# Optimization experiments

Hardware: AMD Instinct MI355X
Metric: run time of the kernel (lower is better)

## Reference

```python
import jax, jax.numpy as jnp
import numpy as np
from jax import lax

C = 256        # shared head channels (out_ch)
NB = 6         # anchors per spatial location
NC = 9         # num_classes (incl. background)
B = 16         # batch
FM = [(38, 38), (19, 19), (10, 10), (5, 5), (3, 3), (1, 1)]
BIAS_PRIOR = -float(np.log((1.0 - 0.01) / 0.01))  # focal-style prior on cls bias


def _conv(x, w, b):
    # 3x3 conv, stride 1, SAME padding, NCHW/OIHW
    y = lax.conv_general_dilated(x, w, (1, 1), 'SAME',
                                 dimension_numbers=('NCHW', 'OIHW', 'NCHW'))
    return y + b[None, :, None, None]


def _head(x, ws, bs):
    for w, b in zip(ws[:-1], bs[:-1]):
        x = jax.nn.relu(_conv(x, w, b))
    return _conv(x, ws[-1], bs[-1])


def setup_inputs() -> dict:
    key = jax.random.key(0)
    ks = jax.random.split(key, 20)
    d = {}
    for i, (h, w) in enumerate(FM):
        d[f'feat{i}'] = jax.random.normal(ks[i], (B, C, h, w), dtype=jnp.float32)
    for i in range(4):
        d[f'rw{i}'] = 0.01 * jax.random.normal(ks[6 + i], (C, C, 3, 3), dtype=jnp.float32)
        d[f'rb{i}'] = jnp.zeros((C,), jnp.float32)
    d['rw4'] = 0.01 * jax.random.normal(ks[10], (NB * 4, C, 3, 3), dtype=jnp.float32)
    d['rb4'] = jnp.zeros((NB * 4,), jnp.float32)
    for i in range(4):
        d[f'cw{i}'] = 0.01 * jax.random.normal(ks[11 + i], (C, C, 3, 3), dtype=jnp.float32)
        d[f'cb{i}'] = jnp.zeros((C,), jnp.float32)
    d['cw4'] = 0.01 * jax.random.normal(ks[15], (NB * NC, C, 3, 3), dtype=jnp.float32)
    cb4 = jnp.zeros((NB * NC,), jnp.float32)
    d['cb4'] = cb4.at[:NB].set(BIAS_PRIOR)  # bias_per_class = n_boxes entries
    return d


def reference(feat0, feat1, feat2, feat3, feat4, feat5,
              rw0, rw1, rw2, rw3, rw4, rb0, rb1, rb2, rb3, rb4,
              cw0, cw1, cw2, cw3, cw4, cb0, cb1, cb2, cb3, cb4):
    feats = [feat0, feat1, feat2, feat3, feat4, feat5]
    rws = [rw0, rw1, rw2, rw3, rw4]
    rbs = [rb0, rb1, rb2, rb3, rb4]
    cws = [cw0, cw1, cw2, cw3, cw4]
    cbs = [cb0, cb1, cb2, cb3, cb4]
    locs, confs = [], []
    for x in feats:
        n = x.shape[0]
        locs.append(_head(x, rws, rbs).reshape(n, 4, -1))       # [N,4,NB*H*W]
        confs.append(_head(x, cws, cbs).reshape(n, NC, -1))     # [N,NC,NB*H*W]
    bbox_delta = jnp.concatenate(locs, axis=2)   # [N, 4, total_anchors]
    confidences = jnp.concatenate(confs, axis=2)  # [N, NC, total_anchors]
    return bbox_delta, confidences
```

## Files before the change

kernel.cpp:

```cpp
#include <hip/hip_runtime.h>
#include <hip/hip_bf16.h>

typedef __attribute__((ext_vector_type(8))) __bf16 bf16x8;
typedef __attribute__((ext_vector_type(4))) float f32x4;

__device__ __forceinline__ unsigned short f2bf(float f) {
    unsigned int u = __float_as_uint(f);
    u += 0x7fff + ((u >> 16) & 1);
    return (unsigned short)(u >> 16);
}

__device__ __forceinline__ void gload16(const void* g, void* l) {
    __builtin_amdgcn_global_load_lds(
        (const __attribute__((address_space(1))) void*)g,
        (__attribute__((address_space(3))) void*)l, 16, 0, 0);
}

#define ZOFFB (31040 * 512)

__device__ __forceinline__ void tile256(int rt, int& rb, int& dim, int& row0) {
    if (rt < 91)       { rb = 0;     dim = 38; row0 = rt * 256; }
    else if (rt < 114) { rb = 23104; dim = 19; row0 = (rt - 91) * 256; }
    else if (rt < 121) { rb = 28880; dim = 10; row0 = (rt - 114) * 256; }
    else if (rt < 123) { rb = 30480; dim = 5;  row0 = (rt - 121) * 256; }
    else if (rt < 124) { rb = 30880; dim = 3;  row0 = (rt - 123) * 256; }
    else               { rb = 31024; dim = 1;  row0 = 0; }
    row0 += rb;
}

__device__ __forceinline__ void tile128(int rt, int& rb, int& dim, int& row0, int& aoff) {
    if (rt < 181)      { rb = 0;     dim = 38; row0 = rt * 128;         aoff = 0;     }
    else if (rt < 227) { rb = 23104; dim = 19; row0 = (rt - 181) * 128; aoff = 8664;  }
    else if (rt < 240) { rb = 28880; dim = 10; row0 = (rt - 227) * 128; aoff = 10830; }
    else if (rt < 244) { rb = 30480; dim = 5;  row0 = (rt - 240) * 128; aoff = 11430; }
    else if (rt < 246) { rb = 30880; dim = 3;  row0 = (rt - 244) * 128; aoff = 11580; }
    else               { rb = 31024; dim = 1;  row0 = (rt - 246) * 128; aoff = 11634; }
    row0 += rb;
}

struct WT { const float* src[10]; };
__global__ __launch_bounds__(256) void wtrans_all(WT wt, unsigned short* __restrict__ Wb,
                                                  unsigned short* __restrict__ WF) {
    int cr = blockIdx.x;
    int ci = threadIdx.x;
    const float* src;
    unsigned short* dst;
    int co, Cout;
    if (cr < 2048) {
        int slot = cr >> 8; co = cr & 255;
        src = wt.src[slot];
        dst = Wb + (size_t)slot * 589824 + (size_t)co * 2304;
        Cout = 256;
    } else {
        int r = cr - 2048;
        int slot = r >> 6; co = r & 63;
        src = wt.src[8 + slot];
        dst = WF + (size_t)slot * 147456 + (size_t)co * 2304;
        Cout = slot ? 54 : 24;
    }
    float v[9];
    if (co < Cout) {
        const float* s = src + (size_t)(co * 256 + ci) * 9;
#pragma unroll
        for (int t = 0; t < 9; ++t) v[t] = s[t];
    } else {
#pragma unroll
        for (int t = 0; t < 9; ++t) v[t] = 0.0f;
    }
#pragma unroll
    for (int t = 0; t < 9; ++t) dst[t * 256 + ci] = f2bf(v[t]);
}

struct FT { const float* src[6]; unsigned short* halo[4]; int nh; };
__global__ void ftrans_all(FT ft, unsigned short* __restrict__ X0) {
    int idx = blockIdx.x * 256 + threadIdx.x;
    if (idx >= 993280) {
        int idx2 = idx - 993280;
        int buf = idx2 >> 8, off = idx2 & 255;
        if (buf < ft.nh) ft.halo[buf][off] = 0;
        return;
    }
    int row = idx >> 5;
    int c8  = (idx & 31) << 3;
    int m, rb, dim;
    if (row < 23104)      { m = 0; rb = 0;     dim = 38; }
    else if (row < 28880) { m = 1; rb = 23104; dim = 19; }
    else if (row < 30480) { m = 2; rb = 28880; dim = 10; }
    else if (row < 30880) { m = 3; rb = 30480; dim = 5;  }
    else if (row < 31024) { m = 4; rb = 30880; dim = 3;  }
    else                  { m = 5; rb = 31024; dim = 1;  }
    int HW = dim * dim;
    int rel = row - rb;
    int b = rel / HW;
    int hw = rel - b * HW;
    const float* s = ft.src[m] + (size_t)(b * 256 + c8) * HW + hw;
    union { unsigned short u[8]; uint4 v; } tmp;
#pragma unroll
    for (int j = 0; j < 8; ++j) tmp.u[j] = f2bf(s[(size_t)j * HW]);
    *reinterpret_cast<uint4*>(X0 + ((size_t)row << 8) + c8) = tmp.v;
}

struct GArgs {
    const unsigned short* X[2];
    const unsigned short* W[2];
    const float* B[2];
    unsigned short* Y[2];
};

__global__ __launch_bounds__(512, 2) void conv_gemm(GArgs ga) {
    __shared__ unsigned char As[65536];
    __shared__ unsigned char Bs[65536];

    const int hz = blockIdx.y;
    const unsigned char* __restrict__ Xb = (const unsigned char*)ga.X[hz];
    const unsigned char* __restrict__ Wt = (const unsigned char*)ga.W[hz];
    const float* __restrict__ bias = ga.B[hz];
    unsigned short* __restrict__ Y = ga.Y[hz];

    int rb, dim, row0;
    tile256(blockIdx.x, rb, dim, row0);
    const int HWm = dim * dim;
    const int rowEnd = rb + 16 * HWm;

    const int tid = threadIdx.x;
    const int lane = tid & 63, wid = tid >> 6;
    const int lr = lane & 15, lg = lane >> 4;
    const int wm = wid >> 2, wn = wid & 3;

    const int sr0 = tid >> 2;
    const int xsw = (((tid & 3) ^ ((sr0 >> 1) & 3)) << 4);
    const unsigned char* Zr = Xb + ZOFFB + xsw;

    int gg[2], ay[2], ax[2];
    bool av[2];
#pragma unroll
    for (int it = 0; it < 2; ++it) {
        int g = row0 + sr0 + it * 128;
        bool v = g < rowEnd;
        int rel = v ? (g - rb) : 0;
        int b = rel / HWm;
        int hw = rel - b * HWm;
        int y = hw / dim;
        gg[it] = g; ay[it] = y; ax[it] = hw - y * dim; av[it] = v;
    }

    const unsigned char* bsrc0 = Wt + (size_t)sr0 * 4608 + xsw;
    const unsigned char* bsrc1 = Wt + (size_t)(sr0 + 128) * 4608 + xsw;

    auto tapA = [&](int tap, const unsigned char*& p0, const unsigned char*& p1) {
        int q3 = tap / 3;
        int dy = q3 - 1, dx = tap - q3 * 3 - 1;
        int ddd = dy * dim + dx;
        bool v0 = av[0] && ((unsigned)(ay[0] + dy) < (unsigned)dim) && ((unsigned)(ax[0] + dx) < (unsigned)dim);
        bool v1 = av[1] && ((unsigned)(ay[1] + dy) < (unsigned)dim) && ((unsigned)(ax[1] + dx) < (unsigned)dim);
        p0 = v0 ? Xb + (size_t)(gg[0] + ddd) * 512 + xsw : Zr;
        p1 = v1 ? Xb + (size_t)(gg[1] + ddd) * 512 + xsw : Zr;
    };

    const int fswz = ((lg ^ ((lr >> 1) & 3)) << 4);
    const int aRd = (wm * 128 + lr) * 64 + fswz;
    const int bRd = (wn * 64 + lr) * 64 + fswz;
    const int dSt = wid * 1024;

    f32x4 acc[8][4];
#pragma unroll
    for (int i = 0; i < 8; ++i)
#pragma unroll
        for (int j = 0; j < 4; ++j) acc[i][j] = (f32x4){0.f, 0.f, 0.f, 0.f};

    const unsigned char *aC0, *aC1, *aN0, *aN1;
    tapA(0, aC0, aC1);
#pragma unroll
    for (int kt = 0; kt < 3; ++kt) {
        gload16(aC0 + kt * 64, As + kt * 16384 + dSt);
        gload16(aC1 + kt * 64, As + kt * 16384 + 8192 + dSt);
        gload16(bsrc0 + kt * 64, Bs + kt * 16384 + dSt);
        gload16(bsrc1 + kt * 64, Bs + kt * 16384 + 8192 + dSt);
    }

#pragma unroll 1
    for (int tap = 0; tap < 9; ++tap) {
        if (tap < 8) tapA(tap + 1, aN0, aN1);
        else { aN0 = Zr; aN1 = Zr; }
        const unsigned char* bT0 = bsrc0 + tap * 512;
        const unsigned char* bT1 = bsrc1 + tap * 512;

#pragma unroll
        for (int kc = 0; kc < 8; ++kc) {
            const int bufc = kc & 3;
            const int bufs = (kc + 3) & 3;

            asm volatile("s_waitcnt vmcnt(8)" ::: "memory");
            __builtin_amdgcn_s_barrier();
            asm volatile("" ::: "memory");

            {
                const unsigned char *sa0, *sa1, *sb0, *sb1;
                if (kc < 5) {
                    sa0 = aC0 + (kc + 3) * 64; sa1 = aC1 + (kc + 3) * 64;
                    sb0 = bT0 + (kc + 3) * 64; sb1 = bT1 + (kc + 3) * 64;
                } else {
                    sa0 = aN0 + (kc - 5) * 64; sa1 = aN1 + (kc - 5) * 64;
                    sb0 = bT0 + 512 + (kc - 5) * 64; sb1 = bT1 + 512 + (kc - 5) * 64;
                }
                gload16(sa0, As + bufs * 16384 + dSt);
                gload16(sa1, As + bufs * 16384 + 8192 + dSt);
                gload16(sb0, Bs + bufs * 16384 + dSt);
                gload16(sb1, Bs + bufs * 16384 + 8192 + dSt);
            }

            const unsigned char* ab = As + bufc * 16384;
            const unsigned char* bb = Bs + bufc * 16384;
            bf16x8 rA[8], rB[4];
#pragma unroll
            for (int j = 0; j < 4; ++j) rB[j] = *(const bf16x8*)(bb + bRd + j * 1024);
#pragma unroll
            for (int i = 0; i < 8; ++i) rA[i] = *(const bf16x8*)(ab + aRd + i * 1024);
#pragma unroll
            for (int i = 0; i < 8; ++i)
#pragma unroll
                for (int j = 0; j < 4; ++j)
                    acc[i][j] = __builtin_amdgcn_mfma_f32_16x16x32_bf16(rA[i], rB[j], acc[i][j], 0, 0, 0);
        }
        aC0 = aN0; aC1 = aN1;
    }

    float bj[4];
#pragma unroll
    for (int j = 0; j < 4; ++j) bj[j] = bias[wn * 64 + j * 16 + lr];
#pragma unroll
    for (int i = 0; i < 8; ++i) {
        int rbase = row0 + wm * 128 + i * 16 + lg * 4;
#pragma unroll
        for (int rr = 0; rr < 4; ++rr) {
            int orow = rbase + rr;
            if (orow < rowEnd) {
                size_t yb = (size_t)orow * 256 + wn * 64 + lr;
#pragma unroll
                for (int j = 0; j < 4; ++j) {
                    float v = acc[i][j][rr] + bj[j];
                    Y[yb + j * 16] = f2bf(fmaxf(v, 0.f));
                }
            }
        }
    }
}

struct FArgs {
    const unsigned short* X[2];
    const unsigned short* W[2];
    const float* B[2];
    float* out;
    int hbase;
};

__global__ __launch_bounds__(256) void conv_final(FArgs fa) {
    __shared__ unsigned char As[32768];
    __shared__ unsigned char Bs[16384];

    const int zi = blockIdx.z;
    const int hz = zi + fa.hbase;
    const unsigned char* Xb = (const unsigned char*)fa.X[zi];
    const unsigned char* Wt = (const unsigned char*)fa.W[zi];
    const float* bias = fa.B[zi];
    float* out = fa.out;

    int rb, dim, row0, aoff;
    tile128(blockIdx.x, rb, dim, row0, aoff);
    const int HWm = dim * dim;
    const int rowEnd = rb + 16 * HWm;

    const int tid = threadIdx.x;
    const int lane = tid & 63, wid = tid >> 6;
    const int lr = lane & 15, lg = lane >> 4;

    const int swz16 = (((lane & 3) ^ ((lane >> 3) & 3)) << 4);
    const int srow = wid * 16 + (lane >> 2);
    const unsigned char* Zr = Xb + ZOFFB + swz16;

    int ay[2], ax[2], arel[2];
    bool av0[2];
#pragma unroll
    for (int it = 0; it < 2; ++it) {
        int r = row0 + it * 64 + srow;
        bool v = r < rowEnd;
        int rel = v ? (r - rb) : 0;
        int b = rel / HWm;
        int hw = rel - b * HWm;
        int y = hw / dim;
        ay[it] = y; ax[it] = hw - y * dim; arel[it] = rel; av0[it] = v;
    }

    const unsigned char* bB = Wt + (size_t)srow * 4608 + swz16;

    const int fsw = ((lg ^ ((lr >> 1) & 3)) << 4);
    const int aRd = (wid * 32 + lr) * 64 + fsw;
    const int bRd = lr * 64 + fsw;
    const int dA0 = wid * 1024;

    f32x4 acc[2][4];
#pragma unroll
    for (int i = 0; i < 2; ++i)
#pragma unroll
        for (int j = 0; j < 4; ++j) acc[i][j] = (f32x4){0.f, 0.f, 0.f, 0.f};

    auto tapPtr = [&](int tap, const unsigned char** aP) {
        int q3 = tap / 3;
        int dy = q3 - 1, dx = tap - q3 * 3 - 1;
#pragma unroll
        for (int it = 0; it < 2; ++it) {
            bool v = av0[it] && ((unsigned)(ay[it] + dy) < (unsigned)dim)
                             && ((unsigned)(ax[it] + dx) < (unsigned)dim);
            int off = v ? (rb + arel[it] + dy * dim + dx) * 512 : ZOFFB;
            aP[it] = Xb + off + swz16;
        }
    };

    const unsigned char* aP[2];
    const unsigned char* aPn[2];
    tapPtr(0, aP);
#pragma unroll
    for (int kt = 0; kt < 3; ++kt) {
        gload16(aP[0] + kt * 64, As + kt * 8192 + dA0);
        gload16(aP[1] + kt * 64, As + kt * 8192 + 4096 + dA0);
        gload16(bB + kt * 64, Bs + kt * 4096 + dA0);
    }

#pragma unroll 1
    for (int tap = 0; tap < 9; ++tap) {
        if (tap < 8) tapPtr(tap + 1, aPn);
        else { aPn[0] = Zr; aPn[1] = Zr; }
        const unsigned char* bP = bB + tap * 512;

#pragma unroll
        for (int kin = 0; kin < 8; ++kin) {
            const int sc = kin & 3;
            const int ss = (kin + 3) & 3;

            asm volatile("s_waitcnt vmcnt(6)" ::: "memory");
            __builtin_amdgcn_s_barrier();
            asm volatile("" ::: "memory");

            {
                const unsigned char *sa0, *sa1, *sb;
                if (tap == 8 && kin >= 5) { sa0 = Zr; sa1 = Zr; sb = Zr; }
                else if (kin < 5) {
                    sa0 = aP[0] + (kin + 3) * 64; sa1 = aP[1] + (kin + 3) * 64;
                    sb = bP + (kin + 3) * 64;
                } else {
                    sa0 = aPn[0] + (kin - 5) * 64; sa1 = aPn[1] + (kin - 5) * 64;
                    sb = bP + 512 + (kin - 5) * 64;
                }
                gload16(sa0, As + ss * 8192 + dA0);
                gload16(sa1, As + ss * 8192 + 4096 + dA0);
                gload16(sb, Bs + ss * 4096 + dA0);
            }

            const unsigned char* ab = As + sc * 8192;
            const unsigned char* bb = Bs + sc * 4096;
            bf16x8 af[2], bg[4];
#pragma unroll
            for (int j = 0; j < 4; ++j) bg[j] = *(const bf16x8*)(bb + bRd + j * 1024);
#pragma unroll
            for (int i = 0; i < 2; ++i) af[i] = *(const bf16x8*)(ab + aRd + i * 1024);
#pragma unroll
            for (int i = 0; i < 2; ++i)
#pragma unroll
                for (int j = 0; j < 4; ++j)
                    acc[i][j] = __builtin_amdgcn_mfma_f32_16x16x32_bf16(af[i], bg[j], acc[i][j], 0, 0, 0);
        }
        aP[0] = aPn[0]; aP[1] = aPn[1];
    }

    const int Cout = hz ? 54 : 24;
#pragma unroll
    for (int i = 0; i < 2; ++i) {
        int rbase = row0 + wid * 32 + i * 16 + lg * 4;
#pragma unroll
        for (int r = 0; r < 4; ++r) {
            int orow = rbase + r;
            if (orow < rowEnd) {
                int rel = orow - rb;
                int b = rel / HWm;
                int hw = rel - b * HWm;
#pragma unroll
                for (int j = 0; j < 4; ++j) {
                    int oc = j * 16 + lr;
                    if (oc < Cout) {
                        int q = oc / 6;
                        int s = oc - q * 6;
                        int anchor = aoff + s * HWm + hw;
                        float v = acc[i][j][r] + bias[oc];
                        if (hz)
                            out[744960 + (size_t)b * 104760 + (size_t)q * 11640 + anchor] = v;
                        else
                            out[(size_t)b * 46560 + (size_t)q * 11640 + anchor] = v;
                    }
                }
            }
        }
    }
}

extern "C" void kernel_launch(void* const* d_in, const int* in_sizes, int n_in,
                              void* d_out, int out_size, void* d_ws, size_t ws_size,
                              hipStream_t stream) {
    (void)in_sizes; (void)n_in; (void)out_size;

    const float* rw[5]  = {(const float*)d_in[6],  (const float*)d_in[8],
                           (const float*)d_in[10], (const float*)d_in[12],
                           (const float*)d_in[14]};
    const float* rbv[5] = {(const float*)d_in[7],  (const float*)d_in[9],
                           (const float*)d_in[11], (const float*)d_in[13],
                           (const float*)d_in[15]};
    const float* cw[5]  = {(const float*)d_in[16], (const float*)d_in[18],
                           (const float*)d_in[20], (const float*)d_in[22],
                           (const float*)d_in[24]};
    const float* cbv[5] = {(const float*)d_in[17], (const float*)d_in[19],
                           (const float*)d_in[21], (const float*)d_in[23],
                           (const float*)d_in[25]};

    const size_t ACTB = 31041ull * 512;
    const size_t WMAT = 589824;
    const size_t WBYTES = 8 * WMAT * 2;
    const size_t WFBYTES = 2 * 147456 * 2;
    const size_t needF = 4 * ACTB + WBYTES + WFBYTES;
    const size_t needS = 3 * ACTB + WBYTES + WFBYTES;

    unsigned char* ws = (unsigned char*)d_ws;
    bool fused = (ws_size >= needF);
    if (!fused && ws_size < needS) return;

    int nact = fused ? 4 : 3;
    unsigned short* act[4];
    for (int i = 0; i < nact; ++i) act[i] = (unsigned short*)(ws + (size_t)i * ACTB);
    unsigned short* Wb = (unsigned short*)(ws + (size_t)nact * ACTB);
    unsigned short* WF = (unsigned short*)(ws + (size_t)nact * ACTB + WBYTES);

    WT wt;
    for (int l = 0; l < 4; ++l) { wt.src[l] = rw[l]; wt.src[4 + l] = cw[l]; }
    wt.src[8] = rw[4]; wt.src[9] = cw[4];
    wtrans_all<<<2176, 256, 0, stream>>>(wt, Wb, WF);

    FT ft;
    for (int i = 0; i < 6; ++i) ft.src[i] = (const float*)d_in[i];
    for (int i = 0; i < 4; ++i)
        ft.halo[i] = (unsigned short*)((unsigned char*)act[i < nact ? i : 0] + ZOFFB);
    ft.nh = nact;
    ftrans_all<<<3884, 256, 0, stream>>>(ft, act[0]);

    const unsigned short* Wr[5], *Wc[5];
    for (int l = 0; l < 4; ++l) {
        Wr[l] = Wb + (size_t)l * WMAT;
        Wc[l] = Wb + (size_t)(4 + l) * WMAT;
    }
    Wr[4] = WF; Wc[4] = WF + 147456;

    if (fused) {
        unsigned short* X0 = act[0];
        unsigned short* P = act[1];
        unsigned short* Q = act[2];
        unsigned short* R = act[3];
        GArgs l1 = {{X0, X0}, {Wr[0], Wc[0]}, {rbv[0], cbv[0]}, {P, Q}};
        GArgs l2 = {{P,  Q},  {Wr[1], Wc[1]}, {rbv[1], cbv[1]}, {X0, R}};
        GArgs l3 = {{X0, R},  {Wr[2], Wc[2]}, {rbv[2], cbv[2]}, {P, Q}};
        GArgs l4 = {{P,  Q},  {Wr[3], Wc[3]}, {rbv[3], cbv[3]}, {X0, R}};
        conv_gemm<<<dim3(125, 2), 512, 0, stream>>>(l1);
        conv_gemm<<<dim3(125, 2), 512, 0, stream>>>(l2);
        conv_gemm<<<dim3(125, 2), 512, 0, stream>>>(l3);
        conv_gemm<<<dim3(125, 2), 512, 0, stream>>>(l4);
        FArgs lf = {{X0, R}, {Wr[4], Wc[4]}, {rbv[4], cbv[4]}, (float*)d_out, 0};
        conv_final<<<dim3(247, 1, 2), 256, 0, stream>>>(lf);
    } else {
        unsigned short* X0 = act[0];
        unsigned short* A1 = act[1];
        unsigned short* A2 = act[2];
        for (int h = 0; h < 2; ++h) {
            const unsigned short* const* W = h ? Wc : Wr;
            const float* const* bs = h ? cbv : rbv;
            GArgs l1 = {{X0, X0}, {W[0], W[0]}, {bs[0], bs[0]}, {A1, A1}};
            GArgs l2 = {{A1, A1}, {W[1], W[1]}, {bs[1], bs[1]}, {A2, A2}};
            GArgs l3 = {{A2, A2}, {W[2], W[2]}, {bs[2], bs[2]}, {A1, A1}};
            GArgs l4 = {{A1, A1}, {W[3], W[3]}, {bs[3], bs[3]}, {A2, A2}};
            conv_gemm<<<dim3(125, 1), 512, 0, stream>>>(l1);
            conv_gemm<<<dim3(125, 1), 512, 0, stream>>>(l2);
            conv_gemm<<<dim3(125, 1), 512, 0, stream>>>(l3);
            conv_gemm<<<dim3(125, 1), 512, 0, stream>>>(l4);
            FArgs lf = {{A2, A2}, {W[4], W[4]}, {bs[4], bs[4]}, (float*)d_out, h};
            conv_final<<<dim3(247, 1, 1), 256, 0, stream>>>(lf);
        }
    }
}
```

Baseline: 373.4 us.

## Load conv weight fragments straight to registers instead of staging in LDS

Weight (B) tiles are no longer copied into shared memory. Each lane now reads its bf16x8 weight fragments directly from global memory into a double-buffered register array, prefetching the next k-chunk while the MFMAs run. This removes the 64 KB B LDS buffer and its LDS reads, which halves the per-block shared memory and may let two blocks share a CU. The cost is uncoalesced, redundant global and L2 weight reads across the waves that share a column tile, extra vector registers, and extra entries in the vmcnt-based pipeline wait.

After: 504.0 us. 35.0% more time.

```diff
diff --git a/kernel.cpp b/kernel.cpp
--- a/kernel.cpp
+++ b/kernel.cpp
@@ -109,7 +109,6 @@
 
 __global__ __launch_bounds__(512, 2) void conv_gemm(GArgs ga) {
     __shared__ unsigned char As[65536];
-    __shared__ unsigned char Bs[65536];
 
     const int hz = blockIdx.y;
     const unsigned char* __restrict__ Xb = (const unsigned char*)ga.X[hz];
@@ -143,9 +142,6 @@
         int y = hw / dim;
         gg[it] = g; ay[it] = y; ax[it] = hw - y * dim; av[it] = v;
     }
-
-    const unsigned char* bsrc0 = Wt + (size_t)sr0 * 4608 + xsw;
-    const unsigned char* bsrc1 = Wt + (size_t)(sr0 + 128) * 4608 + xsw;
 
     auto tapA = [&](int tap, const unsigned char*& p0, const unsigned char*& p1) {
         int q3 = tap / 3;
@@ -157,9 +153,10 @@
         p1 = v1 ? Xb + (size_t)(gg[1] + ddd) * 512 + xsw : Zr;
     };
 
+    const unsigned char* bpt = Wt + (size_t)(wn * 64 + lr) * 4608 + lg * 16;
+
     const int fswz = ((lg ^ ((lr >> 1) & 3)) << 4);
     const int aRd = (wm * 128 + lr) * 64 + fswz;
-    const int bRd = (wn * 64 + lr) * 64 + fswz;
     const int dSt = wid * 1024;
 
     f32x4 acc[8][4];
@@ -167,6 +164,8 @@
     for (int i = 0; i < 8; ++i)
 #pragma unroll
         for (int j = 0; j < 4; ++j) acc[i][j] = (f32x4){0.f, 0.f, 0.f, 0.f};
+
+    bf16x8 bR[2][4];
 
     const unsigned char *aC0, *aC1, *aN0, *aN1;
     tapA(0, aC0, aC1);
@@ -174,53 +173,52 @@
     for (int kt = 0; kt < 3; ++kt) {
         gload16(aC0 + kt * 64, As + kt * 16384 + dSt);
         gload16(aC1 + kt * 64, As + kt * 16384 + 8192 + dSt);
-        gload16(bsrc0 + kt * 64, Bs + kt * 16384 + dSt);
-        gload16(bsrc1 + kt * 64, Bs + kt * 16384 + 8192 + dSt);
-    }
+    }
+#pragma unroll
+    for (int j = 0; j < 4; ++j)
+        bR[0][j] = *(const bf16x8*)(bpt + (size_t)j * 73728);
 
 #pragma unroll 1
     for (int tap = 0; tap < 9; ++tap) {
         if (tap < 8) tapA(tap + 1, aN0, aN1);
         else { aN0 = Zr; aN1 = Zr; }
-        const unsigned char* bT0 = bsrc0 + tap * 512;
-        const unsigned char* bT1 = bsrc1 + tap * 512;
 
 #pragma unroll
         for (int kc = 0; kc < 8; ++kc) {
             const int bufc = kc & 3;
             const int bufs = (kc + 3) & 3;
+            const int pc = kc & 1;
+            const int pn = pc ^ 1;
 
             asm volatile("s_waitcnt vmcnt(8)" ::: "memory");
             __builtin_amdgcn_s_barrier();
             asm volatile("" ::: "memory");
 
             {
-                const unsigned char *sa0, *sa1, *sb0, *sb1;
-                if (kc < 5) {
-                    sa0 = aC0 + (kc + 3) * 64; sa1 = aC1 + (kc + 3) * 64;
-                    sb0 = bT0 + (kc + 3) * 64; sb1 = bT1 + (kc + 3) * 64;
-                } else {
-                    sa0 = aN0 + (kc - 5) * 64; sa1 = aN1 + (kc - 5) * 64;
-                    sb0 = bT0 + 512 + (kc - 5) * 64; sb1 = bT1 + 512 + (kc - 5) * 64;
-                }
+                const unsigned char *sa0, *sa1;
+                if (kc < 5) { sa0 = aC0 + (kc + 3) * 64; sa1 = aC1 + (kc + 3) * 64; }
+                else        { sa0 = aN0 + (kc - 5) * 64; sa1 = aN1 + (kc - 5) * 64; }
                 gload16(sa0, As + bufs * 16384 + dSt);
                 gload16(sa1, As + bufs * 16384 + 8192 + dSt);
-                gload16(sb0, Bs + bufs * 16384 + dSt);
-                gload16(sb1, Bs + bufs * 16384 + 8192 + dSt);
             }
 
+            {
+                const int tn = (tap * 8 + kc + 1) % 72;
+                const int boff = (tn >> 3) * 512 + (tn & 7) * 64;
+#pragma unroll
+                for (int j = 0; j < 4; ++j)
+                    bR[pn][j] = *(const bf16x8*)(bpt + (size_t)j * 73728 + boff);
+            }
+
             const unsigned char* ab = As + bufc * 16384;
-            const unsigned char* bb = Bs + bufc * 16384;
-            bf16x8 rA[8], rB[4];
-#pragma unroll
-            for (int j = 0; j < 4; ++j) rB[j] = *(const bf16x8*)(bb + bRd + j * 1024);
+            bf16x8 rA[8];
 #pragma unroll
             for (int i = 0; i < 8; ++i) rA[i] = *(const bf16x8*)(ab + aRd + i * 1024);
 #pragma unroll
             for (int i = 0; i < 8; ++i)
 #pragma unroll
                 for (int j = 0; j < 4; ++j)
-                    acc[i][j] = __builtin_amdgcn_mfma_f32_16x16x32_bf16(rA[i], rB[j], acc[i][j], 0, 0, 0);
+                    acc[i][j] = __builtin_amdgcn_mfma_f32_16x16x32_bf16(rA[i], bR[pc][j], acc[i][j], 0, 0, 0);
         }
         aC0 = aN0; aC1 = aN1;
     }
```
